# Kernel tuning notes

Hardware: AMD Instinct MI355X
Metric: run time of the kernel (lower is better)

The kernel has to match this reference:

```python
import jax, jax.numpy as jnp
import numpy as np

IN, H, B, T, OUT = 128, 512, 256, 512, 2

def _lstm_layer(x, Wih, Whh, bih, bhh):
    # x: [B, T, D_in] -> h_seq: [B, T, H]. PyTorch gate order: i, f, g, o.
    gx = jnp.einsum('btd,gd->btg', x, Wih) + bih + bhh  # [B, T, 4H]
    gx = jnp.transpose(gx, (1, 0, 2))                    # [T, B, 4H]
    Hh = Whh.shape[1]
    def step(carry, g_t):
        h, c = carry
        g = g_t + h @ Whh.T
        i = jax.nn.sigmoid(g[:, 0*Hh:1*Hh])
        f = jax.nn.sigmoid(g[:, 1*Hh:2*Hh])
        gg = jnp.tanh(g[:, 2*Hh:3*Hh])
        o = jax.nn.sigmoid(g[:, 3*Hh:4*Hh])
        c = f * c + i * gg
        h = o * jnp.tanh(c)
        return (h, c), h
    h0 = jnp.zeros((x.shape[0], Hh), x.dtype)
    (_, _), hs = jax.lax.scan(step, (h0, h0), gx)
    return jnp.transpose(hs, (1, 0, 2))  # [B, T, H]

def setup_inputs() -> dict:
    key = jax.random.key(0)
    ks = jax.random.split(key, 11)
    s = 1.0 / np.sqrt(H)
    u = lambda k, shp: jax.random.uniform(k, shp, jnp.float32, -s, s)
    return {
        'x':    jax.random.normal(ks[0], (B, T, IN), jnp.float32),
        'Wih0': u(ks[1], (4 * H, IN)), 'Whh0': u(ks[2], (4 * H, H)),
        'bih0': u(ks[3], (4 * H,)),    'bhh0': u(ks[4], (4 * H,)),
        'Wih1': u(ks[5], (4 * H, H)),  'Whh1': u(ks[6], (4 * H, H)),
        'bih1': u(ks[7], (4 * H,)),    'bhh1': u(ks[8], (4 * H,)),
        'Wfc':  u(ks[9], (OUT, H)),    'bfc':  u(ks[10], (OUT,)),
    }

def reference(x, Wih0, Whh0, bih0, bhh0, Wih1, Whh1, bih1, bhh1, Wfc, bfc):
    h1 = _lstm_layer(x, Wih0, Whh0, bih0, bhh0)   # layer 0
    h2 = _lstm_layer(h1, Wih1, Whh1, bih1, bhh1)  # layer 1
    return h2[:, -1, :] @ Wfc.T + bfc             # [B, OUT]
```

## Files before the change

kernel.cpp:

```cpp
#include <hip/hip_runtime.h>

#define IN_DIM 128
#define HID    512
#define BATCH  256
#define SEQT   512
#define G4H    2048
#define K0     640
#define K1     1024
#define NC0    20
#define NC1    32
#define ROWB   2048

typedef __attribute__((ext_vector_type(8))) short bf16x8;
typedef __attribute__((ext_vector_type(4))) float f32x4;

#define MFMA16 __builtin_amdgcn_mfma_f32_16x16x32_bf16
#define GL(r, g, c) ((r) * 132 + (g) * 33 + (c))

__device__ __forceinline__ unsigned short f2bf(float f) {
  unsigned u = __float_as_uint(f);
  u += 0x7fffu + ((u >> 16) & 1u);
  return (unsigned short)(u >> 16);
}
__device__ __forceinline__ float bf2f(unsigned short s) {
  return __uint_as_float(((unsigned)s) << 16);
}
__device__ __forceinline__ float sigm(float x) { return 1.0f / (1.0f + __expf(-x)); }
__device__ __forceinline__ float tanh_f(float x) {
  float xc = fminf(fmaxf(x, -15.0f), 15.0f);
  float e = __expf(2.0f * xc);
  return (e - 1.0f) / (e + 1.0f);
}

__device__ __forceinline__ unsigned ald(const unsigned* p) {
  return __hip_atomic_load(p, __ATOMIC_RELAXED, __HIP_MEMORY_SCOPE_AGENT);
}

__global__ void conv_weights(const float* __restrict__ Wih0, const float* __restrict__ Whh0,
                             const float* __restrict__ Wih1, const float* __restrict__ Whh1,
                             const float* __restrict__ bih0, const float* __restrict__ bhh0,
                             const float* __restrict__ bih1, const float* __restrict__ bhh1,
                             short* __restrict__ W0h, short* __restrict__ W0l,
                             short* __restrict__ W1h, short* __restrict__ W1l,
                             float* __restrict__ bsum0, float* __restrict__ bsum1) {
  int idx = blockIdx.x * blockDim.x + threadIdx.x;
  const int N0 = G4H * K0, N1 = G4H * K1;
  if (idx < N0) {
    int tile = idx / (K0 * 16), rem = idx % (K0 * 16);
    int kcg = rem >> 9, l = (rem >> 3) & 63, j = rem & 7;
    int slice = tile >> 2, g = tile & 3;
    int c = l & 15, k = kcg * 32 + ((l >> 4) << 3) + j;
    int n = g * HID + slice * 16 + c;
    float w = (k < IN_DIM) ? Wih0[n * IN_DIM + k] : Whh0[n * HID + (k - IN_DIM)];
    unsigned short hi = f2bf(w);
    W0h[idx] = (short)hi;
    W0l[idx] = (short)f2bf(w - bf2f(hi));
  } else if (idx < N0 + N1) {
    int d = idx - N0;
    int tile = d / (K1 * 16), rem = d % (K1 * 16);
    int kcg = rem >> 9, l = (rem >> 3) & 63, j = rem & 7;
    int slice = tile >> 2, g = tile & 3;
    int c = l & 15, k = kcg * 32 + ((l >> 4) << 3) + j;
    int n = g * HID + slice * 16 + c;
    float w = (k < HID) ? Wih1[n * HID + k] : Whh1[n * HID + (k - HID)];
    unsigned short hi = f2bf(w);
    W1h[d] = (short)hi;
    W1l[d] = (short)f2bf(w - bf2f(hi));
  } else if (idx < N0 + N1 + G4H) {
    int n = idx - (N0 + N1);
    bsum0[n] = bih0[n] + bhh0[n];
  } else if (idx < N0 + N1 + 2 * G4H) {
    int n = idx - (N0 + N1 + G4H);
    bsum1[n] = bih1[n] + bhh1[n];
  }
}

#define PKH(a, b) ((unsigned)((a) & 0xffffu) | (((b) & 0xffffu) << 16))
#define PKL(a, b) (((a) >> 16) | ((b) & 0xffff0000u))

__device__ __forceinline__ void unpack16(char* bh, char* bl, int byte0, int rx,
                                         const uint4& v0, const uint4& v1,
                                         const uint4& v2, const uint4& v3) {
  int4 h0 = {(int)PKH(v0.x, v0.y), (int)PKH(v0.z, v0.w), (int)PKH(v1.x, v1.y), (int)PKH(v1.z, v1.w)};
  int4 h1 = {(int)PKH(v2.x, v2.y), (int)PKH(v2.z, v2.w), (int)PKH(v3.x, v3.y), (int)PKH(v3.z, v3.w)};
  int4 l0 = {(int)PKL(v0.x, v0.y), (int)PKL(v0.z, v0.w), (int)PKL(v1.x, v1.y), (int)PKL(v1.z, v1.w)};
  int4 l1 = {(int)PKL(v2.x, v2.y), (int)PKL(v2.z, v2.w), (int)PKL(v3.x, v3.y), (int)PKL(v3.z, v3.w)};
  *(int4*)(bh + (byte0 ^ rx)) = h0;
  *(int4*)(bh + ((byte0 + 16) ^ rx)) = h1;
  *(int4*)(bl + (byte0 ^ rx)) = l0;
  *(int4*)(bl + ((byte0 + 16) ^ rx)) = l1;
}

__device__ __forceinline__ void stage_one(char* AhiB, char* AloB,
                                          const unsigned* __restrict__ plane,
                                          int b0, int colOff, int tid) {
  const int row = tid >> 5, c32 = tid & 31;
  const unsigned* p = plane + (size_t)(b0 + row) * HID + c32 * 16;
  uint4 v0, v1, v2, v3;
  asm volatile(
      "global_load_dwordx4 %0, %4, off sc0 sc1\n\t"
      "global_load_dwordx4 %1, %4, off offset:16 sc0 sc1\n\t"
      "global_load_dwordx4 %2, %4, off offset:32 sc0 sc1\n\t"
      "global_load_dwordx4 %3, %4, off offset:48 sc0 sc1\n\t"
      "s_waitcnt vmcnt(0)"
      : "=&v"(v0), "=&v"(v1), "=&v"(v2), "=&v"(v3)
      : "v"(p)
      : "memory");
  const int rx = (row & 7) << 4;
  unpack16(AhiB + row * ROWB, AloB + row * ROWB, (colOff + c32 * 16) * 2, rx, v0, v1, v2, v3);
}

__device__ __forceinline__ void stage_two(char* AhiB, char* AloB,
                                          const unsigned* __restrict__ pA,
                                          const unsigned* __restrict__ pB,
                                          int b0, int tid) {
  const int row = tid >> 5, c32 = tid & 31;
  const unsigned* p0 = pA + (size_t)(b0 + row) * HID + c32 * 16;
  const unsigned* p2 = pB + (size_t)(b0 + row) * HID + c32 * 16;
  uint4 v0, v1, v2, v3, w0, w1, w2, w3;
  asm volatile(
      "global_load_dwordx4 %0, %8, off sc0 sc1\n\t"
      "global_load_dwordx4 %1, %8, off offset:16 sc0 sc1\n\t"
      "global_load_dwordx4 %2, %8, off offset:32 sc0 sc1\n\t"
      "global_load_dwordx4 %3, %8, off offset:48 sc0 sc1\n\t"
      "global_load_dwordx4 %4, %9, off sc0 sc1\n\t"
      "global_load_dwordx4 %5, %9, off offset:16 sc0 sc1\n\t"
      "global_load_dwordx4 %6, %9, off offset:32 sc0 sc1\n\t"
      "global_load_dwordx4 %7, %9, off offset:48 sc0 sc1\n\t"
      "s_waitcnt vmcnt(0)"
      : "=&v"(v0), "=&v"(v1), "=&v"(v2), "=&v"(v3),
        "=&v"(w0), "=&v"(w1), "=&v"(w2), "=&v"(w3)
      : "v"(p0), "v"(p2)
      : "memory");
  const int rx = (row & 7) << 4;
  char* bh = AhiB + row * ROWB;
  char* bl = AloB + row * ROWB;
  unpack16(bh, bl, (c32 * 16) * 2, rx, v0, v1, v2, v3);
  unpack16(bh, bl, (HID + c32 * 16) * 2, rx, w0, w1, w2, w3);
}
#undef PKH
#undef PKL

template <int NKC>
__device__ __forceinline__ void gemm32(const char* Ah, const char* Al,
                                       const short* __restrict__ Bh0, const short* __restrict__ Bl0,
                                       const short* __restrict__ Bh1, const short* __restrict__ Bl1,
                                       int lane, int aoff,
                                       f32x4& a00, f32x4& a01, f32x4& a10, f32x4& a11) {
  const int row = lane & 15;
  const int ko  = (lane >> 4) * 8;
  const int rx  = (row & 7) << 4;
  const char* pAh0 = Ah + row * ROWB;
  const char* pAh1 = Ah + (row + 16) * ROWB;
  const char* pAl0 = Al + row * ROWB;
  const char* pAl1 = Al + (row + 16) * ROWB;
#pragma unroll
  for (int kc = 0; kc < NKC; ++kc) {
    const int off = ((aoff + kc * 32 + ko) * 2) ^ rx;
    bf16x8 ah0 = *(const bf16x8*)(pAh0 + off);
    bf16x8 ah1 = *(const bf16x8*)(pAh1 + off);
    bf16x8 al0 = *(const bf16x8*)(pAl0 + off);
    bf16x8 al1 = *(const bf16x8*)(pAl1 + off);
    bf16x8 bh0 = *(const bf16x8*)(Bh0 + kc * 512 + lane * 8);
    bf16x8 bl0 = *(const bf16x8*)(Bl0 + kc * 512 + lane * 8);
    bf16x8 bh1 = *(const bf16x8*)(Bh1 + kc * 512 + lane * 8);
    bf16x8 bl1 = *(const bf16x8*)(Bl1 + kc * 512 + lane * 8);
    a00 = MFMA16(ah0, bh0, a00, 0, 0, 0);
    a01 = MFMA16(ah1, bh0, a01, 0, 0, 0);
    a00 = MFMA16(ah0, bl0, a00, 0, 0, 0);
    a01 = MFMA16(ah1, bl0, a01, 0, 0, 0);
    a00 = MFMA16(al0, bh0, a00, 0, 0, 0);
    a01 = MFMA16(al1, bh0, a01, 0, 0, 0);
    a10 = MFMA16(ah0, bh1, a10, 0, 0, 0);
    a11 = MFMA16(ah1, bh1, a11, 0, 0, 0);
    a10 = MFMA16(ah0, bl1, a10, 0, 0, 0);
    a11 = MFMA16(ah1, bl1, a11, 0, 0, 0);
    a10 = MFMA16(al0, bh1, a10, 0, 0, 0);
    a11 = MFMA16(al1, bh1, a11, 0, 0, 0);
  }
}

__device__ __forceinline__ void finq32(float* glf, int g, int lane,
                                       const f32x4& a00, const f32x4& a01,
                                       const f32x4& a10, const f32x4& a11) {
  const int col = lane & 15;
  const int r0  = (lane >> 4) * 4;
#pragma unroll
  for (int r = 0; r < 4; ++r) {
    atomicAdd(glf + GL(r0 + r, g, col), a00[r]);
    atomicAdd(glf + GL(16 + r0 + r, g, col), a01[r]);
    atomicAdd(glf + GL(r0 + r, g, col + 16), a10[r]);
    atomicAdd(glf + GL(16 + r0 + r, g, col + 16), a11[r]);
  }
}

__device__ __forceinline__ void group_barrier(unsigned* flags, unsigned target,
                                              int tid) {
  asm volatile("s_waitcnt vmcnt(0)" ::: "memory");
  __syncthreads();
  if (tid < 64) {
    if (tid == 0)
      __hip_atomic_store(flags + (int)(blockIdx.x & 31), target,
                         __ATOMIC_RELAXED, __HIP_MEMORY_SCOPE_AGENT);
    const int i = tid & 31;
    while (true) {
      unsigned v = ald(flags + i);
      if (__all((int)(v >= target))) break;
      __builtin_amdgcn_s_sleep(1);
    }
  }
  __syncthreads();
}

__global__ void __launch_bounds__(1024, 4) lstm_fused(
    const float* __restrict__ x,
    const float* __restrict__ Wfc, const float* __restrict__ bfc,
    const short* __restrict__ W0h, const short* __restrict__ W0l,
    const short* __restrict__ W1h, const short* __restrict__ W1l,
    const float* __restrict__ bsum0, const float* __restrict__ bsum1,
    unsigned* __restrict__ h0s, unsigned* __restrict__ h2s,
    unsigned* __restrict__ counters,
    float* __restrict__ out) {
  const int tid  = threadIdx.x;
  const int wv   = tid >> 6;
  const int lane = tid & 63;
  const int wid  = blockIdx.x & 31;
  const int grp  = blockIdx.x >> 5;
  const int role = wid >> 4;
  const int w16  = wid & 15;
  const int hid0 = w16 * 32;
  const int b0   = grp * 32;
  unsigned* flags = counters + grp * 64;

  __shared__ __align__(16) char AhiB[32 * ROWB];
  __shared__ __align__(16) char AloB[32 * ROWB];
  __shared__ float glf[32 * 132];

  const int g  = wv & 3;
  const int kq = wv >> 2;
  const int t0 = (w16 * 2) * 4 + g, t1 = t0 + 4;
  const short *Bh0, *Bl0, *Bh1, *Bl1;
  int aoff;
  if (role == 0) {
    Bh0 = W0h + ((size_t)t0 * NC0 + (size_t)kq * 5) * 512;
    Bl0 = W0l + ((size_t)t0 * NC0 + (size_t)kq * 5) * 512;
    Bh1 = W0h + ((size_t)t1 * NC0 + (size_t)kq * 5) * 512;
    Bl1 = W0l + ((size_t)t1 * NC0 + (size_t)kq * 5) * 512;
    aoff = kq * 160;
  } else {
    Bh0 = W1h + ((size_t)t0 * NC1 + (size_t)kq * 8) * 512;
    Bl0 = W1l + ((size_t)t0 * NC1 + (size_t)kq * 8) * 512;
    Bh1 = W1h + ((size_t)t1 * NC1 + (size_t)kq * 8) * 512;
    Bl1 = W1l + ((size_t)t1 * NC1 + (size_t)kq * 8) * 512;
    aoff = kq * 256;
  }

  float c = 0.f;
  float bs[4];
  {
    const int n = hid0 + (tid & 31);
    const float* bsp = role ? bsum1 : bsum0;
#pragma unroll
    for (int q = 0; q < 4; ++q) bs[q] = bsp[q * HID + n];
  }
  for (int i = tid; i < 32 * 132; i += 1024) glf[i] = 0.f;

  const size_t PL = (size_t)BATCH * HID;

  for (int s = 0; s <= SEQT; ++s) {
    const int cur = s & 1, prv = cur ^ 1;
    unsigned* h0c = h0s + (size_t)cur * PL;
    const unsigned* h0p = h0s + (size_t)prv * PL;
    unsigned* h2c = h2s + (size_t)cur * PL;
    const unsigned* h2p = h2s + (size_t)prv * PL;
    const bool active = role ? (s > 0) : (s < SEQT);

    if (active) {
      if (role == 0) {
        {
          const int row = tid >> 5, t32 = tid & 31;
          const int rx = (row & 7) << 4;
          const float* xs = x + ((size_t)(b0 + row) * SEQT + s) * IN_DIM + t32 * 4;
          float4 xv = *(const float4*)xs;
          unsigned short h0v = f2bf(xv.x), h1v = f2bf(xv.y), h2v = f2bf(xv.z), h3v = f2bf(xv.w);
          uint2 hd = {(unsigned)h0v | ((unsigned)h1v << 16), (unsigned)h2v | ((unsigned)h3v << 16)};
          uint2 ld = {(unsigned)f2bf(xv.x - bf2f(h0v)) | ((unsigned)f2bf(xv.y - bf2f(h1v)) << 16),
                      (unsigned)f2bf(xv.z - bf2f(h2v)) | ((unsigned)f2bf(xv.w - bf2f(h3v)) << 16)};
          const int byte = (t32 * 8) ^ rx;
          *(uint2*)(AhiB + row * ROWB + byte) = hd;
          *(uint2*)(AloB + row * ROWB + byte) = ld;
        }
        stage_one(AhiB, AloB, h0p, b0, IN_DIM, tid);
      } else {
        stage_two(AhiB, AloB, h0p, h2p, b0, tid);
      }
    }
    __syncthreads();

    if (active) {
      f32x4 a00 = {0.f, 0.f, 0.f, 0.f}, a01 = {0.f, 0.f, 0.f, 0.f};
      f32x4 a10 = {0.f, 0.f, 0.f, 0.f}, a11 = {0.f, 0.f, 0.f, 0.f};
      if (role == 0)
        gemm32<5>(AhiB, AloB, Bh0, Bl0, Bh1, Bl1, lane, aoff, a00, a01, a10, a11);
      else
        gemm32<8>(AhiB, AloB, Bh0, Bl0, Bh1, Bl1, lane, aoff, a00, a01, a10, a11);
      finq32(glf, g, lane, a00, a01, a10, a11);
    }
    __syncthreads();

    if (active) {
      const int row = tid >> 5, col = tid & 31;
      float gi = glf[GL(row, 0, col)] + bs[0];
      float gf = glf[GL(row, 1, col)] + bs[1];
      float gg = glf[GL(row, 2, col)] + bs[2];
      float go = glf[GL(row, 3, col)] + bs[3];
      glf[GL(row, 0, col)] = 0.f; glf[GL(row, 1, col)] = 0.f;
      glf[GL(row, 2, col)] = 0.f; glf[GL(row, 3, col)] = 0.f;
      float i = sigm(gi), f = sigm(gf), gv = tanh_f(gg), o = sigm(go);
      float cc = f * c + i * gv;
      c = cc;
      float h = o * tanh_f(cc);
      unsigned short hh = f2bf(h);
      unsigned short hl = f2bf(h - bf2f(hh));
      unsigned pk = (unsigned)hh | ((unsigned)hl << 16);
      unsigned* hc = role ? h2c : h0c;
      __hip_atomic_store(hc + (size_t)(b0 + row) * HID + hid0 + col, pk,
                         __ATOMIC_RELAXED, __HIP_MEMORY_SCOPE_AGENT);
    }

    group_barrier(flags, (unsigned)(s + 1), tid);
  }

  {
    const int p = tid >> 3, q = tid & 7;
    float acc = 0.f;
    if (wid == 0 && tid < 512) {
      const int b = b0 + (p >> 1), o = p & 1;
      const unsigned* sp = h2s + (size_t)b * HID + q * 64;
      const float* wf = Wfc + (size_t)o * HID + q * 64;
#pragma unroll 8
      for (int i = 0; i < 64; ++i) {
        unsigned u = ald(sp + i);
        acc += (bf2f((unsigned short)(u & 0xffff)) + bf2f((unsigned short)(u >> 16))) * wf[i];
      }
      glf[p * 8 + q] = acc;
    }
    __syncthreads();
    if (wid == 0 && tid < 512 && q == 0) {
      float t = 0.f;
#pragma unroll
      for (int i = 0; i < 8; ++i) t += glf[p * 8 + i];
      out[(b0 + (p >> 1)) * 2 + (p & 1)] = t + bfc[p & 1];
    }
  }
}

extern "C" void kernel_launch(void* const* d_in, const int* in_sizes, int n_in,
                              void* d_out, int out_size, void* d_ws, size_t ws_size,
                              hipStream_t stream) {
  const float* x    = (const float*)d_in[0];
  const float* Wih0 = (const float*)d_in[1];
  const float* Whh0 = (const float*)d_in[2];
  const float* bih0 = (const float*)d_in[3];
  const float* bhh0 = (const float*)d_in[4];
  const float* Wih1 = (const float*)d_in[5];
  const float* Whh1 = (const float*)d_in[6];
  const float* bih1 = (const float*)d_in[7];
  const float* bhh1 = (const float*)d_in[8];
  const float* Wfc  = (const float*)d_in[9];
  const float* bfc  = (const float*)d_in[10];
  float* out = (float*)d_out;

  short* W0h = (short*)d_ws;
  short* W0l = W0h + (size_t)G4H * K0;
  short* W1h = W0l + (size_t)G4H * K0;
  short* W1l = W1h + (size_t)G4H * K1;
  unsigned* h0s = (unsigned*)(W1l + (size_t)G4H * K1);
  unsigned* h2s = h0s + (size_t)2 * BATCH * HID;
  unsigned* counters = h2s + (size_t)2 * BATCH * HID;
  float* bsum0 = (float*)(counters + 512);
  float* bsum1 = bsum0 + G4H;

  (void)hipMemsetAsync(h0s, 0,
                       (size_t)4 * BATCH * HID * sizeof(unsigned) + 512 * sizeof(unsigned),
                       stream);

  const int total = G4H * K0 + G4H * K1 + 2 * G4H;
  conv_weights<<<(total + 255) / 256, 256, 0, stream>>>(
      Wih0, Whh0, Wih1, Whh1, bih0, bhh0, bih1, bhh1,
      W0h, W0l, W1h, W1l, bsum0, bsum1);

  void* args[] = {(void*)&x,    (void*)&Wfc,  (void*)&bfc,
                  (void*)&W0h,  (void*)&W0l,  (void*)&W1h, (void*)&W1l,
                  (void*)&bsum0, (void*)&bsum1,
                  (void*)&h0s,  (void*)&h2s,  (void*)&counters, (void*)&out};
  (void)hipLaunchCooperativeKernel((void*)lstm_fused, dim3(256), dim3(1024), args, 0,
                                   stream);
}
```

Measured before the change: 16.93 ms.

## Repartition LSTM work into 16-row batch groups with 64-wide hidden slices

Reshapes the cooperative decomposition. Each block now handles 16 batch rows and 64 hidden units instead of 32 rows and 32 units, so 16 groups of 16 blocks run instead of 8 groups of 32. The GEMM now loads one A fragment and reuses it across four B tiles, and staging and barrier code are rewritten to match. The aim is cheaper per-group barriers with fewer participants and better A reuse, at the cost of more B-weight traffic per block and smaller M tiles per MFMA.

```diff
diff --git a/kernel.cpp b/kernel.cpp
--- a/kernel.cpp
+++ b/kernel.cpp
@@ -9,13 +9,14 @@
 #define K1     1024
 #define NC0    20
 #define NC1    32
+#define GR     16
 #define ROWB   2048
 
 typedef __attribute__((ext_vector_type(8))) short bf16x8;
 typedef __attribute__((ext_vector_type(4))) float f32x4;
 
 #define MFMA16 __builtin_amdgcn_mfma_f32_16x16x32_bf16
-#define GL(r, g, c) ((r) * 132 + (g) * 33 + (c))
+#define GL(r, g, c) ((r) * 264 + (g) * 66 + (c))
 
 __device__ __forceinline__ unsigned short f2bf(float f) {
   unsigned u = __float_as_uint(f);
@@ -78,131 +79,129 @@
 #define PKH(a, b) ((unsigned)((a) & 0xffffu) | (((b) & 0xffffu) << 16))
 #define PKL(a, b) (((a) >> 16) | ((b) & 0xffff0000u))
 
-__device__ __forceinline__ void unpack16(char* bh, char* bl, int byte0, int rx,
-                                         const uint4& v0, const uint4& v1,
-                                         const uint4& v2, const uint4& v3) {
-  int4 h0 = {(int)PKH(v0.x, v0.y), (int)PKH(v0.z, v0.w), (int)PKH(v1.x, v1.y), (int)PKH(v1.z, v1.w)};
-  int4 h1 = {(int)PKH(v2.x, v2.y), (int)PKH(v2.z, v2.w), (int)PKH(v3.x, v3.y), (int)PKH(v3.z, v3.w)};
-  int4 l0 = {(int)PKL(v0.x, v0.y), (int)PKL(v0.z, v0.w), (int)PKL(v1.x, v1.y), (int)PKL(v1.z, v1.w)};
-  int4 l1 = {(int)PKL(v2.x, v2.y), (int)PKL(v2.z, v2.w), (int)PKL(v3.x, v3.y), (int)PKL(v3.z, v3.w)};
-  *(int4*)(bh + (byte0 ^ rx)) = h0;
-  *(int4*)(bh + ((byte0 + 16) ^ rx)) = h1;
-  *(int4*)(bl + (byte0 ^ rx)) = l0;
-  *(int4*)(bl + ((byte0 + 16) ^ rx)) = l1;
-}
-
-__device__ __forceinline__ void stage_one(char* AhiB, char* AloB,
-                                          const unsigned* __restrict__ plane,
-                                          int b0, int colOff, int tid) {
-  const int row = tid >> 5, c32 = tid & 31;
-  const unsigned* p = plane + (size_t)(b0 + row) * HID + c32 * 16;
-  uint4 v0, v1, v2, v3;
+__device__ __forceinline__ void unpack_chunk(char* AhiB, char* AloB, int colOff,
+                                             int c, const uint4& v) {
+  const int row  = c >> 7;
+  const int colb = (c & 127) * 4;
+  const int rx   = (row & 7) << 4;
+  const int byte0 = (colOff + colb) * 2;
+  uint2 hd = {PKH(v.x, v.y), PKH(v.z, v.w)};
+  uint2 ld = {PKL(v.x, v.y), PKL(v.z, v.w)};
+  *(uint2*)(AhiB + row * ROWB + (byte0 ^ rx)) = hd;
+  *(uint2*)(AloB + row * ROWB + (byte0 ^ rx)) = ld;
+}
+
+__device__ __forceinline__ void stage_L0(char* AhiB, char* AloB,
+                                         const unsigned* __restrict__ h0p,
+                                         int b0, int tid) {
+  const unsigned* pb = h0p + (size_t)b0 * HID;
+  const unsigned* a0 = pb + tid * 4;
+  const unsigned* a1 = a0 + 4096;
+  uint4 v0, v1;
+  asm volatile(
+      "global_load_dwordx4 %0, %2, off sc0 sc1\n\t"
+      "global_load_dwordx4 %1, %3, off sc0 sc1\n\t"
+      "s_waitcnt vmcnt(0)"
+      : "=&v"(v0), "=&v"(v1)
+      : "v"(a0), "v"(a1)
+      : "memory");
+  unpack_chunk(AhiB, AloB, IN_DIM, tid, v0);
+  unpack_chunk(AhiB, AloB, IN_DIM, tid + 1024, v1);
+}
+
+__device__ __forceinline__ void stage_L1(char* AhiB, char* AloB,
+                                         const unsigned* __restrict__ h0p,
+                                         const unsigned* __restrict__ h2p,
+                                         int b0, int tid) {
+  const unsigned* pa = h0p + (size_t)b0 * HID;
+  const unsigned* pb = h2p + (size_t)b0 * HID;
+  const unsigned* a0 = pa + tid * 4;
+  const unsigned* a1 = a0 + 4096;
+  const unsigned* b0p = pb + tid * 4;
+  const unsigned* b1p = b0p + 4096;
+  uint4 v0, v1, w0, w1;
   asm volatile(
       "global_load_dwordx4 %0, %4, off sc0 sc1\n\t"
-      "global_load_dwordx4 %1, %4, off offset:16 sc0 sc1\n\t"
-      "global_load_dwordx4 %2, %4, off offset:32 sc0 sc1\n\t"
-      "global_load_dwordx4 %3, %4, off offset:48 sc0 sc1\n\t"
+      "global_load_dwordx4 %1, %5, off sc0 sc1\n\t"
+      "global_load_dwordx4 %2, %6, off sc0 sc1\n\t"
+      "global_load_dwordx4 %3, %7, off sc0 sc1\n\t"
       "s_waitcnt vmcnt(0)"
-      : "=&v"(v0), "=&v"(v1), "=&v"(v2), "=&v"(v3)
-      : "v"(p)
+      : "=&v"(v0), "=&v"(v1), "=&v"(w0), "=&v"(w1)
+      : "v"(a0), "v"(a1), "v"(b0p), "v"(b1p)
       : "memory");
-  const int rx = (row & 7) << 4;
-  unpack16(AhiB + row * ROWB, AloB + row * ROWB, (colOff + c32 * 16) * 2, rx, v0, v1, v2, v3);
-}
-
-__device__ __forceinline__ void stage_two(char* AhiB, char* AloB,
-                                          const unsigned* __restrict__ pA,
-                                          const unsigned* __restrict__ pB,
-                                          int b0, int tid) {
-  const int row = tid >> 5, c32 = tid & 31;
-  const unsigned* p0 = pA + (size_t)(b0 + row) * HID + c32 * 16;
-  const unsigned* p2 = pB + (size_t)(b0 + row) * HID + c32 * 16;
-  uint4 v0, v1, v2, v3, w0, w1, w2, w3;
-  asm volatile(
-      "global_load_dwordx4 %0, %8, off sc0 sc1\n\t"
-      "global_load_dwordx4 %1, %8, off offset:16 sc0 sc1\n\t"
-      "global_load_dwordx4 %2, %8, off offset:32 sc0 sc1\n\t"
-      "global_load_dwordx4 %3, %8, off offset:48 sc0 sc1\n\t"
-      "global_load_dwordx4 %4, %9, off sc0 sc1\n\t"
-      "global_load_dwordx4 %5, %9, off offset:16 sc0 sc1\n\t"
-      "global_load_dwordx4 %6, %9, off offset:32 sc0 sc1\n\t"
-      "global_load_dwordx4 %7, %9, off offset:48 sc0 sc1\n\t"
-      "s_waitcnt vmcnt(0)"
-      : "=&v"(v0), "=&v"(v1), "=&v"(v2), "=&v"(v3),
-        "=&v"(w0), "=&v"(w1), "=&v"(w2), "=&v"(w3)
-      : "v"(p0), "v"(p2)
-      : "memory");
-  const int rx = (row & 7) << 4;
-  char* bh = AhiB + row * ROWB;
-  char* bl = AloB + row * ROWB;
-  unpack16(bh, bl, (c32 * 16) * 2, rx, v0, v1, v2, v3);
-  unpack16(bh, bl, (HID + c32 * 16) * 2, rx, w0, w1, w2, w3);
+  unpack_chunk(AhiB, AloB, 0, tid, v0);
+  unpack_chunk(AhiB, AloB, 0, tid + 1024, v1);
+  unpack_chunk(AhiB, AloB, HID, tid, w0);
+  unpack_chunk(AhiB, AloB, HID, tid + 1024, w1);
 }
 #undef PKH
 #undef PKL
 
 template <int NKC>
-__device__ __forceinline__ void gemm32(const char* Ah, const char* Al,
+__device__ __forceinline__ void gemm64(const char* Ah, const char* Al,
                                        const short* __restrict__ Bh0, const short* __restrict__ Bl0,
                                        const short* __restrict__ Bh1, const short* __restrict__ Bl1,
+                                       const short* __restrict__ Bh2, const short* __restrict__ Bl2,
+                                       const short* __restrict__ Bh3, const short* __restrict__ Bl3,
                                        int lane, int aoff,
-                                       f32x4& a00, f32x4& a01, f32x4& a10, f32x4& a11) {
+                                       f32x4& c0, f32x4& c1, f32x4& c2, f32x4& c3) {
   const int row = lane & 15;
   const int ko  = (lane >> 4) * 8;
   const int rx  = (row & 7) << 4;
-  const char* pAh0 = Ah + row * ROWB;
-  const char* pAh1 = Ah + (row + 16) * ROWB;
-  const char* pAl0 = Al + row * ROWB;
-  const char* pAl1 = Al + (row + 16) * ROWB;
+  const char* pAh = Ah + row * ROWB;
+  const char* pAl = Al + row * ROWB;
 #pragma unroll
   for (int kc = 0; kc < NKC; ++kc) {
     const int off = ((aoff + kc * 32 + ko) * 2) ^ rx;
-    bf16x8 ah0 = *(const bf16x8*)(pAh0 + off);
-    bf16x8 ah1 = *(const bf16x8*)(pAh1 + off);
-    bf16x8 al0 = *(const bf16x8*)(pAl0 + off);
-    bf16x8 al1 = *(const bf16x8*)(pAl1 + off);
-    bf16x8 bh0 = *(const bf16x8*)(Bh0 + kc * 512 + lane * 8);
-    bf16x8 bl0 = *(const bf16x8*)(Bl0 + kc * 512 + lane * 8);
-    bf16x8 bh1 = *(const bf16x8*)(Bh1 + kc * 512 + lane * 8);
-    bf16x8 bl1 = *(const bf16x8*)(Bl1 + kc * 512 + lane * 8);
-    a00 = MFMA16(ah0, bh0, a00, 0, 0, 0);
-    a01 = MFMA16(ah1, bh0, a01, 0, 0, 0);
-    a00 = MFMA16(ah0, bl0, a00, 0, 0, 0);
-    a01 = MFMA16(ah1, bl0, a01, 0, 0, 0);
-    a00 = MFMA16(al0, bh0, a00, 0, 0, 0);
-    a01 = MFMA16(al1, bh0, a01, 0, 0, 0);
-    a10 = MFMA16(ah0, bh1, a10, 0, 0, 0);
-    a11 = MFMA16(ah1, bh1, a11, 0, 0, 0);
-    a10 = MFMA16(ah0, bl1, a10, 0, 0, 0);
-    a11 = MFMA16(ah1, bl1, a11, 0, 0, 0);
-    a10 = MFMA16(al0, bh1, a10, 0, 0, 0);
-    a11 = MFMA16(al1, bh1, a11, 0, 0, 0);
-  }
-}
-
-__device__ __forceinline__ void finq32(float* glf, int g, int lane,
-                                       const f32x4& a00, const f32x4& a01,
-                                       const f32x4& a10, const f32x4& a11) {
+    bf16x8 ah = *(const bf16x8*)(pAh + off);
+    bf16x8 al = *(const bf16x8*)(pAl + off);
+    const int bo = kc * 512 + lane * 8;
+    bf16x8 bh0 = *(const bf16x8*)(Bh0 + bo);
+    bf16x8 bl0 = *(const bf16x8*)(Bl0 + bo);
+    bf16x8 bh1 = *(const bf16x8*)(Bh1 + bo);
+    bf16x8 bl1 = *(const bf16x8*)(Bl1 + bo);
+    bf16x8 bh2 = *(const bf16x8*)(Bh2 + bo);
+    bf16x8 bl2 = *(const bf16x8*)(Bl2 + bo);
+    bf16x8 bh3 = *(const bf16x8*)(Bh3 + bo);
+    bf16x8 bl3 = *(const bf16x8*)(Bl3 + bo);
+    c0 = MFMA16(ah, bh0, c0, 0, 0, 0);
+    c0 = MFMA16(ah, bl0, c0, 0, 0, 0);
+    c0 = MFMA16(al, bh0, c0, 0, 0, 0);
+    c1 = MFMA16(ah, bh1, c1, 0, 0, 0);
+    c1 = MFMA16(ah, bl1, c1, 0, 0, 0);
+    c1 = MFMA16(al, bh1, c1, 0, 0, 0);
+    c2 = MFMA16(ah, bh2, c2, 0, 0, 0);
+    c2 = MFMA16(ah, bl2, c2, 0, 0, 0);
+    c2 = MFMA16(al, bh2, c2, 0, 0, 0);
+    c3 = MFMA16(ah, bh3, c3, 0, 0, 0);
+    c3 = MFMA16(ah, bl3, c3, 0, 0, 0);
+    c3 = MFMA16(al, bh3, c3, 0, 0, 0);
+  }
+}
+
+__device__ __forceinline__ void finq(float* glf, int g, int lane,
+                                     const f32x4& c0, const f32x4& c1,
+                                     const f32x4& c2, const f32x4& c3) {
   const int col = lane & 15;
   const int r0  = (lane >> 4) * 4;
 #pragma unroll
   for (int r = 0; r < 4; ++r) {
-    atomicAdd(glf + GL(r0 + r, g, col), a00[r]);
-    atomicAdd(glf + GL(16 + r0 + r, g, col), a01[r]);
-    atomicAdd(glf + GL(r0 + r, g, col + 16), a10[r]);
-    atomicAdd(glf + GL(16 + r0 + r, g, col + 16), a11[r]);
+    atomicAdd(glf + GL(r0 + r, g, col), c0[r]);
+    atomicAdd(glf + GL(r0 + r, g, 16 + col), c1[r]);
+    atomicAdd(glf + GL(r0 + r, g, 32 + col), c2[r]);
+    atomicAdd(glf + GL(r0 + r, g, 48 + col), c3[r]);
   }
 }
 
 __device__ __forceinline__ void group_barrier(unsigned* flags, unsigned target,
-                                              int tid) {
+                                              int tid, int wid) {
   asm volatile("s_waitcnt vmcnt(0)" ::: "memory");
   __syncthreads();
   if (tid < 64) {
     if (tid == 0)
-      __hip_atomic_store(flags + (int)(blockIdx.x & 31), target,
-                         __ATOMIC_RELAXED, __HIP_MEMORY_SCOPE_AGENT);
-    const int i = tid & 31;
+      __hip_atomic_store(flags + wid, target, __ATOMIC_RELAXED,
+                         __HIP_MEMORY_SCOPE_AGENT);
+    const int i = tid & 15;
     while (true) {
       unsigned v = ald(flags + i);
       if (__all((int)(v >= target))) break;
@@ -224,46 +223,51 @@
   const int tid  = threadIdx.x;
   const int wv   = tid >> 6;
   const int lane = tid & 63;
-  const int wid  = blockIdx.x & 31;
-  const int grp  = blockIdx.x >> 5;
-  const int role = wid >> 4;
-  const int w16  = wid & 15;
-  const int hid0 = w16 * 32;
-  const int b0   = grp * 32;
+  const int wid  = blockIdx.x & 15;
+  const int grp  = blockIdx.x >> 4;
+  const int role = wid >> 3;
+  const int w8   = wid & 7;
+  const int hid0 = w8 * 64;
+  const int b0   = grp * GR;
   unsigned* flags = counters + grp * 64;
 
-  __shared__ __align__(16) char AhiB[32 * ROWB];
-  __shared__ __align__(16) char AloB[32 * ROWB];
-  __shared__ float glf[32 * 132];
+  __shared__ __align__(16) char AhiB[GR * ROWB];
+  __shared__ __align__(16) char AloB[GR * ROWB];
+  __shared__ float glf[16 * 264];
 
   const int g  = wv & 3;
   const int kq = wv >> 2;
-  const int t0 = (w16 * 2) * 4 + g, t1 = t0 + 4;
-  const short *Bh0, *Bl0, *Bh1, *Bl1;
+  const short *Bh0, *Bl0, *Bh1, *Bl1, *Bh2, *Bl2, *Bh3, *Bl3;
   int aoff;
   if (role == 0) {
-    Bh0 = W0h + ((size_t)t0 * NC0 + (size_t)kq * 5) * 512;
-    Bl0 = W0l + ((size_t)t0 * NC0 + (size_t)kq * 5) * 512;
-    Bh1 = W0h + ((size_t)t1 * NC0 + (size_t)kq * 5) * 512;
-    Bl1 = W0l + ((size_t)t1 * NC0 + (size_t)kq * 5) * 512;
+    const size_t base = (size_t)kq * 5 * 512;
+#define T0(i) ((size_t)((w8 * 4 + (i)) * 4 + g) * NC0 * 512 + base)
+    Bh0 = W0h + T0(0); Bl0 = W0l + T0(0);
+    Bh1 = W0h + T0(1); Bl1 = W0l + T0(1);
+    Bh2 = W0h + T0(2); Bl2 = W0l + T0(2);
+    Bh3 = W0h + T0(3); Bl3 = W0l + T0(3);
+#undef T0
     aoff = kq * 160;
   } else {
-    Bh0 = W1h + ((size_t)t0 * NC1 + (size_t)kq * 8) * 512;
-    Bl0 = W1l + ((size_t)t0 * NC1 + (size_t)kq * 8) * 512;
-    Bh1 = W1h + ((size_t)t1 * NC1 + (size_t)kq * 8) * 512;
-    Bl1 = W1l + ((size_t)t1 * NC1 + (size_t)kq * 8) * 512;
+    const size_t base = (size_t)kq * 8 * 512;
+#define T1(i) ((size_t)((w8 * 4 + (i)) * 4 + g) * NC1 * 512 + base)
+    Bh0 = W1h + T1(0); Bl0 = W1l + T1(0);
+    Bh1 = W1h + T1(1); Bl1 = W1l + T1(1);
+    Bh2 = W1h + T1(2); Bl2 = W1l + T1(2);
+    Bh3 = W1h + T1(3); Bl3 = W1l + T1(3);
+#undef T1
     aoff = kq * 256;
   }
 
   float c = 0.f;
   float bs[4];
   {
-    const int n = hid0 + (tid & 31);
+    const int n = hid0 + (tid & 63);
     const float* bsp = role ? bsum1 : bsum0;
 #pragma unroll
     for (int q = 0; q < 4; ++q) bs[q] = bsp[q * HID + n];
   }
-  for (int i = tid; i < 32 * 132; i += 1024) glf[i] = 0.f;
+  for (int i = tid; i < 16 * 264; i += 1024) glf[i] = 0.f;
 
   const size_t PL = (size_t)BATCH * HID;
 
@@ -278,38 +282,39 @@
     if (active) {
       if (role == 0) {
         {
-          const int row = tid >> 5, t32 = tid & 31;
+          const int row = wv, l = lane;
           const int rx = (row & 7) << 4;
-          const float* xs = x + ((size_t)(b0 + row) * SEQT + s) * IN_DIM + t32 * 4;
-          float4 xv = *(const float4*)xs;
-          unsigned short h0v = f2bf(xv.x), h1v = f2bf(xv.y), h2v = f2bf(xv.z), h3v = f2bf(xv.w);
-          uint2 hd = {(unsigned)h0v | ((unsigned)h1v << 16), (unsigned)h2v | ((unsigned)h3v << 16)};
-          uint2 ld = {(unsigned)f2bf(xv.x - bf2f(h0v)) | ((unsigned)f2bf(xv.y - bf2f(h1v)) << 16),
-                      (unsigned)f2bf(xv.z - bf2f(h2v)) | ((unsigned)f2bf(xv.w - bf2f(h3v)) << 16)};
-          const int byte = (t32 * 8) ^ rx;
-          *(uint2*)(AhiB + row * ROWB + byte) = hd;
-          *(uint2*)(AloB + row * ROWB + byte) = ld;
+          const float2 xv = *(const float2*)(x + ((size_t)(b0 + row) * SEQT + s) * IN_DIM + l * 2);
+          unsigned short h0v = f2bf(xv.x), h1v = f2bf(xv.y);
+          unsigned hd = (unsigned)h0v | ((unsigned)h1v << 16);
+          unsigned ld = (unsigned)f2bf(xv.x - bf2f(h0v)) |
+                        ((unsigned)f2bf(xv.y - bf2f(h1v)) << 16);
+          const int byte = (l * 4) ^ rx;
+          *(unsigned*)(AhiB + row * ROWB + byte) = hd;
+          *(unsigned*)(AloB + row * ROWB + byte) = ld;
         }
-        stage_one(AhiB, AloB, h0p, b0, IN_DIM, tid);
+        stage_L0(AhiB, AloB, h0p, b0, tid);
       } else {
-        stage_two(AhiB, AloB, h0p, h2p, b0, tid);
+        stage_L1(AhiB, AloB, h0p, h2p, b0, tid);
       }
     }
     __syncthreads();
 
     if (active) {
-      f32x4 a00 = {0.f, 0.f, 0.f, 0.f}, a01 = {0.f, 0.f, 0.f, 0.f};
-      f32x4 a10 = {0.f, 0.f, 0.f, 0.f}, a11 = {0.f, 0.f, 0.f, 0.f};
+      f32x4 c0 = {0.f, 0.f, 0.f, 0.f}, c1 = {0.f, 0.f, 0.f, 0.f};
+      f32x4 c2 = {0.f, 0.f, 0.f, 0.f}, c3 = {0.f, 0.f, 0.f, 0.f};
       if (role == 0)
-        gemm32<5>(AhiB, AloB, Bh0, Bl0, Bh1, Bl1, lane, aoff, a00, a01, a10, a11);
+        gemm64<5>(AhiB, AloB, Bh0, Bl0, Bh1, Bl1, Bh2, Bl2, Bh3, Bl3,
+                  lane, aoff, c0, c1, c2, c3);
       else
-        gemm32<8>(AhiB, AloB, Bh0, Bl0, Bh1, Bl1, lane, aoff, a00, a01, a10, a11);
-      finq32(glf, g, lane, a00, a01, a10, a11);
+        gemm64<8>(AhiB, AloB, Bh0, Bl0, Bh1, Bl1, Bh2, Bl2, Bh3, Bl3,
+                  lane, aoff, c0, c1, c2, c3);
+      finq(glf, g, lane, c0, c1, c2, c3);
     }
     __syncthreads();
 
     if (active) {
-      const int row = tid >> 5, col = tid & 31;
+      const int row = tid >> 6, col = tid & 63;
       float gi = glf[GL(row, 0, col)] + bs[0];
       float gf = glf[GL(row, 1, col)] + bs[1];
       float gg = glf[GL(row, 2, col)] + bs[2];
@@ -328,28 +333,28 @@
                          __ATOMIC_RELAXED, __HIP_MEMORY_SCOPE_AGENT);
     }
 
-    group_barrier(flags, (unsigned)(s + 1), tid);
+    group_barrier(flags, (unsigned)(s + 1), tid, wid);
   }
 
   {
-    const int p = tid >> 3, q = tid & 7;
+    const int p = tid >> 4, q = tid & 15;
     float acc = 0.f;
     if (wid == 0 && tid < 512) {
       const int b = b0 + (p >> 1), o = p & 1;
-      const unsigned* sp = h2s + (size_t)b * HID + q * 64;
-      const float* wf = Wfc + (size_t)o * HID + q * 64;
+      const unsigned* sp = h2s + (size_t)b * HID + q * 32;
+      const float* wf = Wfc + (size_t)o * HID + q * 32;
 #pragma unroll 8
-      for (int i = 0; i < 64; ++i) {
+      for (int i = 0; i < 32; ++i) {
         unsigned u = ald(sp + i);
         acc += (bf2f((unsigned short)(u & 0xffff)) + bf2f((unsigned short)(u >> 16))) * wf[i];
       }
-      glf[p * 8 + q] = acc;
+      glf[p * 16 + q] = acc;
     }
     __syncthreads();
     if (wid == 0 && tid < 512 && q == 0) {
       float t = 0.f;
 #pragma unroll
-      for (int i = 0; i < 8; ++i) t += glf[p * 8 + i];
+      for (int i = 0; i < 16; ++i) t += glf[p * 16 + i];
       out[(b0 + (p >> 1)) * 2 + (p & 1)] = t + bfc[p & 1];
     }
   }
@@ -378,11 +383,11 @@
   unsigned* h0s = (unsigned*)(W1l + (size_t)G4H * K1);
   unsigned* h2s = h0s + (size_t)2 * BATCH * HID;
   unsigned* counters = h2s + (size_t)2 * BATCH * HID;
-  float* bsum0 = (float*)(counters + 512);
+  float* bsum0 = (float*)(counters + 1024);
   float* bsum1 = bsum0 + G4H;
 
   (void)hipMemsetAsync(h0s, 0,
-                       (size_t)4 * BATCH * HID * sizeof(unsigned) + 512 * sizeof(unsigned),
+                       (size_t)4 * BATCH * HID * sizeof(unsigned) + 1024 * sizeof(unsigned),
                        stream);
 
   const int total = G4H * K0 + G4H * K1 + 2 * G4H;
```

Measured after the change: 20.49 ms. 1.21x slower.
